# Kernel tuning notes

Measured on AMD Instinct MI355X. Metric: run time of the kernel, lower is better.

## Reference

```python
import jax, jax.numpy as jnp
import numpy as np

N_EMBD = 1024
N_HEAD = 16
HEAD = N_EMBD // N_HEAD


def setup_inputs() -> dict:
    key = jax.random.key(0)
    ks = jax.random.split(key, 5)
    B, T = 2, 2048
    s = 1.0 / np.sqrt(N_EMBD)
    return {
        "x": jax.random.normal(ks[0], (B, T, N_EMBD), jnp.float32),
        "w_attn": jax.random.normal(ks[1], (N_EMBD, 3 * N_EMBD), jnp.float32) * s,
        "b_attn": jnp.zeros((3 * N_EMBD,), jnp.float32),
        "w_proj": jax.random.normal(ks[2], (N_EMBD, N_EMBD), jnp.float32) * s,
        "b_proj": jnp.zeros((N_EMBD,), jnp.float32),
    }


def reference(x, w_attn, b_attn, w_proj, b_proj):
    B, T, C = x.shape
    qkv = x @ w_attn + b_attn                      # [B,T,3C]
    q, k, v = jnp.split(qkv, 3, axis=-1)
    def heads(t):
        return t.reshape(B, T, N_HEAD, HEAD).transpose(0, 2, 1, 3)  # [B,H,T,D]
    q, k, v = heads(q), heads(k), heads(v)
    scale = 1.0 / np.sqrt(HEAD)
    att = jnp.einsum('bhqd,bhkd->bhqk', q, k) * scale
    causal = jnp.tril(jnp.ones((T, T), bool))
    att = jnp.where(causal, att, -jnp.inf)
    p = jax.nn.softmax(att, axis=-1)
    y = jnp.einsum('bhqk,bhkd->bhqd', p, v)        # [B,H,T,D]
    y = y.transpose(0, 2, 1, 3).reshape(B, T, C)
    return y @ w_proj + b_proj
```

## Files before the change

### kernel.cpp

```cpp
#include <hip/hip_runtime.h>
#include <hip/hip_bf16.h>

typedef __attribute__((ext_vector_type(4))) float f32x4;
typedef __attribute__((ext_vector_type(16))) float f32x16;
typedef __attribute__((ext_vector_type(8))) short bf16x8;
typedef __attribute__((ext_vector_type(4))) unsigned int u32x4;

#define MFMA16(a,b,c) __builtin_amdgcn_mfma_f32_16x16x32_bf16(a,b,c,0,0,0)
#define MFMA32(a,b,c) __builtin_amdgcn_mfma_f32_32x32x16_bf16(a,b,c,0,0,0)
#define LOG2E 1.44269504088896340736f

__device__ __forceinline__ float bf2f(unsigned short u){
  unsigned v = ((unsigned)u) << 16;
  float f; __builtin_memcpy(&f, &v, 4); return f;
}
__device__ __forceinline__ unsigned short f2bf(float f){
  unsigned x; __builtin_memcpy(&x, &f, 4);
  x += 0x7fffu + ((x >> 16) & 1u);
  return (unsigned short)(x >> 16);
}
__device__ __forceinline__ void gload_lds16(const void* g, void* l){
  __builtin_amdgcn_global_load_lds((const __attribute__((address_space(1))) void*)g,
                                   (__attribute__((address_space(3))) void*)l, 16, 0, 0);
}
__device__ __forceinline__ f32x16 zero16(){
  f32x16 z;
#pragma unroll
  for (int i = 0; i < 16; ++i) z[i] = 0.f;
  return z;
}
__device__ __forceinline__ unsigned cvtpk(float lo, float hi_){
  unsigned d;
  asm("v_cvt_pk_bf16_f32 %0, %1, %2" : "=v"(d) : "v"(lo), "v"(hi_));
  return d;
}
__device__ __forceinline__ void pack_group(const float* p, bf16x8& f0, bf16x8& f1){
  unsigned a0 = cvtpk(p[0], p[1]),  b0 = cvtpk(p[4],  p[5]);
  unsigned a1 = cvtpk(p[2], p[3]),  b1 = cvtpk(p[6],  p[7]);
  unsigned c0 = cvtpk(p[8], p[9]),  d0 = cvtpk(p[12], p[13]);
  unsigned c1 = cvtpk(p[10],p[11]), d1 = cvtpk(p[14], p[15]);
  asm("v_permlane32_swap_b32 %0, %1" : "+v"(a0), "+v"(b0));
  asm("v_permlane32_swap_b32 %0, %1" : "+v"(a1), "+v"(b1));
  asm("v_permlane32_swap_b32 %0, %1" : "+v"(c0), "+v"(d0));
  asm("v_permlane32_swap_b32 %0, %1" : "+v"(c1), "+v"(d1));
  u32x4 w0 = {a0, a1, b0, b1};
  u32x4 w1 = {c0, c1, d0, d1};
  f0 = __builtin_bit_cast(bf16x8, w0);
  f1 = __builtin_bit_cast(bf16x8, w1);
}

__global__ void k_cast(const float* __restrict__ src, unsigned short* __restrict__ dst){
  const int i = blockIdx.x * 256 + threadIdx.x;
  const float4 v = ((const float4*)src)[i];
  ushort4 o;
  o.x = f2bf(v.x); o.y = f2bf(v.y); o.z = f2bf(v.z); o.w = f2bf(v.w);
  ((ushort4*)dst)[i] = o;
}

__global__ void k_castT(const float* __restrict__ src, unsigned short* __restrict__ dst,
                        const int R, const int C){
  __shared__ unsigned short t[64][65];
  const int r0 = blockIdx.y * 64, c0 = blockIdx.x * 64;
  const int tid = threadIdx.x;
#pragma unroll
  for (int i = 0; i < 16; ++i){
    int idx = i*256 + tid; int r = idx >> 6, c = idx & 63;
    t[r][c] = f2bf(src[(size_t)(r0 + r)*C + c0 + c]);
  }
  __syncthreads();
#pragma unroll
  for (int i = 0; i < 16; ++i){
    int idx = i*256 + tid; int c = idx >> 6, r = idx & 63;
    dst[(size_t)(c0 + c)*R + r0 + r] = t[r][c];
  }
}

__device__ __forceinline__ void gemm_core3(const unsigned short* __restrict__ A,
                                           const unsigned short* __restrict__ Bt,
                                           const int K, const int bm, const int bn,
                                           char* ldsb, f32x4 acc[4][4])
{
  const int tid = threadIdx.x, lane = tid & 63, wave = tid >> 6;
  const int wr = wave >> 1, wc = wave & 1;
  const int l15 = lane & 15, lg = lane >> 4;
  const int o = tid * 16;
  const int srow = o >> 6;
  const int sch = ((o >> 4) & 3) ^ ((srow >> 1) & 3);
  const unsigned short* gA0 = A  + (size_t)(bm + srow)*K      + sch*8;
  const unsigned short* gA1 = A  + (size_t)(bm + 64 + srow)*K + sch*8;
  const unsigned short* gB0 = Bt + (size_t)(bn + srow)*K      + sch*8;
  const unsigned short* gB1 = Bt + (size_t)(bn + 64 + srow)*K + sch*8;
  const int rsw = (l15 >> 1) & 3;
  const int aoff = (wr*64 + l15)*64 + ((lg ^ rsw) << 4);
  const int boff = 8192 + (wc*64 + l15)*64 + ((lg ^ rsw) << 4);

#define STG3(koff, bb) do { \
    gload_lds16(gA0 + (koff), ldsb + (bb) + o); \
    gload_lds16(gA1 + (koff), ldsb + (bb) + 4096 + o); \
    gload_lds16(gB0 + (koff), ldsb + (bb) + 8192 + o); \
    gload_lds16(gB1 + (koff), ldsb + (bb) + 12288 + o); } while(0)

  const int NT = K >> 5;
  STG3(0, 0);
  STG3(32, 16384);
  int bcur = 0, bstg = 32768;
  for (int t = 0; t < NT; ++t){
    if (t + 1 < NT) asm volatile("s_waitcnt vmcnt(4)" ::: "memory");
    else            asm volatile("s_waitcnt vmcnt(0)" ::: "memory");
    __builtin_amdgcn_s_barrier();
    __builtin_amdgcn_sched_barrier(0);
    if (t + 2 < NT) STG3((size_t)(t + 2) << 5, bstg);
    bf16x8 af[4], bg[4];
#pragma unroll
    for (int m = 0; m < 4; ++m) af[m] = *(const bf16x8*)(ldsb + bcur + aoff + m*1024);
#pragma unroll
    for (int n = 0; n < 4; ++n) bg[n] = *(const bf16x8*)(ldsb + bcur + boff + n*1024);
    __builtin_amdgcn_s_setprio(1);
#pragma unroll
    for (int m = 0; m < 4; ++m)
#pragma unroll
      for (int n = 0; n < 4; ++n)
        acc[m][n] = MFMA16(af[m], bg[n], acc[m][n]);
    __builtin_amdgcn_s_setprio(0);
    bcur = (bcur == 32768) ? 0 : bcur + 16384;
    bstg = (bstg == 32768) ? 0 : bstg + 16384;
  }
#undef STG3
}

__global__ __launch_bounds__(256,3) void k_gemm_qkv(const unsigned short* __restrict__ xb,
    const unsigned short* __restrict__ waT, const float* __restrict__ b_attn,
    unsigned short* __restrict__ qb, unsigned short* __restrict__ kb,
    unsigned short* __restrict__ vb)
{
  __shared__ char lds[49152];
  f32x4 acc[4][4];
#pragma unroll
  for (int m = 0; m < 4; ++m)
#pragma unroll
    for (int n = 0; n < 4; ++n) acc[m][n] = (f32x4){0.f,0.f,0.f,0.f};
  int wgid = blockIdx.y * 24 + blockIdx.x;
  wgid = (wgid & 7) * 96 + (wgid >> 3);
  const int bm = (wgid / 24) * 128, bn = (wgid % 24) * 128;
  gemm_core3(xb, waT, 1024, bm, bn, lds, acc);
  const int lane = threadIdx.x & 63, wave = threadIdx.x >> 6;
  const int wr = wave >> 1, wc = wave & 1, l15 = lane & 15, lg = lane >> 4;
#pragma unroll
  for (int m = 0; m < 4; ++m){
#pragma unroll
    for (int n = 0; n < 4; ++n){
#pragma unroll
      for (int r = 0; r < 4; ++r){
        const int row = bm + wr*64 + m*16 + lg*4 + r;
        const int col = bn + wc*64 + n*16 + l15;
        const float val = acc[m][n][r] + b_attn[col];
        const int part = col >> 10, c = col & 1023;
        const int h = c >> 6, d = c & 63;
        const int b = row >> 11, t = row & 2047;
        const unsigned short u = f2bf(val);
        const size_t bhbase = (size_t)(b*16 + h)*131072;
        if (part == 0){
          qb[bhbase + (size_t)t*64 + d] = u;
        } else {
          const int tile = t >> 6, l = t & 63;
          const size_t base = bhbase + (size_t)tile*4096;
          if (part == 1) kb[base + l*64 + ((((d>>3)^(l&7))<<3) | (d&7))] = u;
          else           vb[base + d*64 + ((((l>>3)^(d&7))<<3) | (l&7))] = u;
        }
      }
    }
  }
}

__global__ __launch_bounds__(256,3) void k_gemm_proj(const unsigned short* __restrict__ yb,
    const unsigned short* __restrict__ wpT, const float* __restrict__ b_proj,
    float* __restrict__ out)
{
  __shared__ char lds[49152];
  f32x4 acc[4][4];
#pragma unroll
  for (int m = 0; m < 4; ++m)
#pragma unroll
    for (int n = 0; n < 4; ++n) acc[m][n] = (f32x4){0.f,0.f,0.f,0.f};
  int wgid = blockIdx.y * 8 + blockIdx.x;
  wgid = (wgid & 7) * 32 + (wgid >> 3);
  const int bm = (wgid / 8) * 128, bn = (wgid % 8) * 128;
  gemm_core3(yb, wpT, 1024, bm, bn, lds, acc);
  const int lane = threadIdx.x & 63, wave = threadIdx.x >> 6;
  const int wr = wave >> 1, wc = wave & 1, l15 = lane & 15, lg = lane >> 4;
#pragma unroll
  for (int m = 0; m < 4; ++m){
#pragma unroll
    for (int n = 0; n < 4; ++n){
#pragma unroll
      for (int r = 0; r < 4; ++r){
        const int row = bm + wr*64 + m*16 + lg*4 + r;
        const int col = bn + wc*64 + n*16 + l15;
        out[(size_t)row*1024 + col] = acc[m][n][r] + b_proj[col];
      }
    }
  }
}

__global__ __launch_bounds__(256,2) void k_attn(const unsigned short* __restrict__ q,
                       const unsigned short* __restrict__ kt,
                       const unsigned short* __restrict__ vt,
                       unsigned short* __restrict__ y)
{
  __shared__ char lds[32768];
  const int tid = threadIdx.x, lane = tid & 63, wave = tid >> 6;
  const int l31 = lane & 31, hi = lane >> 5;
  const int i = blockIdx.x, ii = i & 255;
  const int bh = ii & 31;
  const int qbi = (i < 256) ? (15 - (ii >> 5)) : (ii >> 5);
  const int q0w = qbi*128 + wave*32;
  const int ntiles = (qbi + 1) * 2;
  const unsigned short* qh = q + (size_t)bh * 131072;
  const char* kbase = (const char*)(kt + (size_t)bh * 131072);
  const char* vbase = (const char*)(vt + (size_t)bh * 131072);

  const float C = 0.125f * LOG2E;
  const float M = 16.0f;

  bf16x8 qf[4];
  {
    const unsigned short* qp = qh + (size_t)(q0w + l31)*64 + hi*8;
#pragma unroll
    for (int ds = 0; ds < 4; ++ds) qf[ds] = *(const bf16x8*)(qp + ds*16);
  }

  f32x16 yac0 = zero16(), yac1 = zero16();
  float lsum = 0.f;
  const int mask_from = q0w >> 6;
  const int stg = tid * 16;
  const int dst = wave * 1024;
  char* ldsK = lds;
  char* ldsV = lds + 16384;

#define STAGE(tile, buf) do { \
    const char* ks_ = kbase + (size_t)(tile)*8192; \
    const char* vs_ = vbase + (size_t)(tile)*8192; \
    gload_lds16(ks_ + stg,        ldsK + (buf)*8192 + dst); \
    gload_lds16(ks_ + 4096 + stg, ldsK + (buf)*8192 + 4096 + dst); \
    gload_lds16(vs_ + stg,        ldsV + (buf)*8192 + dst); \
    gload_lds16(vs_ + 4096 + stg, ldsV + (buf)*8192 + 4096 + dst); \
  } while(0)

  STAGE(0, 0);
  __syncthreads();

  const int swz = (l31 & 7) << 4;
  const int rowb = l31 * 128;

  for (int t = 0; t < ntiles; ++t){
    const int buf = t & 1;
    if (t + 1 < ntiles) STAGE(t + 1, buf ^ 1);

    const char* kb_ = ldsK + buf*8192;
    const char* vb_ = ldsV + buf*8192;

    bf16x8 kf[8];
#pragma unroll
    for (int ds = 0; ds < 4; ++ds){
      const int ch = ((ds*2 + hi) << 4) ^ swz;
      kf[ds]   = *(const bf16x8*)(kb_ + rowb + ch);
      kf[ds+4] = *(const bf16x8*)(kb_ + 4096 + rowb + ch);
    }
    f32x16 s0 = zero16(), s1 = zero16();
#pragma unroll
    for (int ds = 0; ds < 4; ++ds){
      s0 = MFMA32(kf[ds],   qf[ds], s0);
      s1 = MFMA32(kf[ds+4], qf[ds], s1);
    }

    bf16x8 vf[8];
#pragma unroll
    for (int ks = 0; ks < 4; ++ks){
      const int ch = ((ks*2 + hi) << 4) ^ swz;
      vf[ks]   = *(const bf16x8*)(vb_ + rowb + ch);
      vf[ks+4] = *(const bf16x8*)(vb_ + 4096 + rowb + ch);
    }

    if (t >= mask_from){
      const int qg = q0w + l31, key0 = t << 6;
#pragma unroll
      for (int r = 0; r < 16; ++r){
        const int kl = (r&3) + 8*(r>>2) + 4*hi;
        if (key0 + kl      > qg) s0[r] = -1e30f;
        if (key0 + 32 + kl > qg) s1[r] = -1e30f;
      }
    }

    float p0[16], p1[16];
    float ts = 0.f;
#pragma unroll
    for (int r = 0; r < 16; ++r){
      p0[r] = __builtin_amdgcn_exp2f(__builtin_fmaf(s0[r], C, -M));
      p1[r] = __builtin_amdgcn_exp2f(__builtin_fmaf(s1[r], C, -M));
      ts += p0[r] + p1[r];
    }
    lsum += ts;

    bf16x8 pa[4];
    pack_group(p0, pa[0], pa[1]);
    pack_group(p1, pa[2], pa[3]);
#pragma unroll
    for (int ks = 0; ks < 4; ++ks){
      yac0 = MFMA32(pa[ks], vf[ks],   yac0);
      yac1 = MFMA32(pa[ks], vf[ks+4], yac1);
    }
    __syncthreads();
  }
#undef STAGE

  lsum += __shfl_xor(lsum, 32);
  const float linv = 1.0f / lsum;
  const int b = bh >> 4, h = bh & 15;
  unsigned short* yp = y + ((size_t)b*2048 + q0w)*1024 + h*64;
#pragma unroll
  for (int r = 0; r < 16; ++r){
    const int ql = (r&3) + 8*(r>>2) + 4*hi;
    const float li = __shfl(linv, ql);
    yp[(size_t)ql*1024 + l31]      = f2bf(yac0[r] * li);
    yp[(size_t)ql*1024 + 32 + l31] = f2bf(yac1[r] * li);
  }
}

extern "C" void kernel_launch(void* const* d_in, const int* in_sizes, int n_in,
                              void* d_out, int out_size, void* d_ws, size_t ws_size,
                              hipStream_t stream) {
  const float* x      = (const float*)d_in[0];
  const float* w_attn = (const float*)d_in[1];
  const float* b_attn = (const float*)d_in[2];
  const float* w_proj = (const float*)d_in[3];
  const float* b_proj = (const float*)d_in[4];
  float* out = (float*)d_out;

  unsigned short* ws  = (unsigned short*)d_ws;
  unsigned short* xb  = ws;
  unsigned short* waT = xb  + 4194304;
  unsigned short* wpT = waT + 3145728;
  unsigned short* qb  = wpT + 1048576;
  unsigned short* kb  = qb  + 4194304;
  unsigned short* vb  = kb  + 4194304;
  unsigned short* yb  = vb  + 4194304;

  k_cast<<<dim3(4096), dim3(256), 0, stream>>>(x, xb);
  k_castT<<<dim3(48,16), dim3(256), 0, stream>>>(w_attn, waT, 1024, 3072);
  k_castT<<<dim3(16,16), dim3(256), 0, stream>>>(w_proj, wpT, 1024, 1024);
  k_gemm_qkv<<<dim3(24,32), dim3(256), 0, stream>>>(xb, waT, b_attn, qb, kb, vb);
  k_attn<<<dim3(512), dim3(256), 0, stream>>>(qb, kb, vb, yb);
  k_gemm_proj<<<dim3(8,32), dim3(256), 0, stream>>>(yb, wpT, b_proj, out);
}
```

Measured before the change: 101.0 us.

## Rewrite QKV GEMM with 256x256 tiles, 8 waves, and interleaved staging

Replaces the 128x128 QKV GEMM, which used 4 waves and 3 blocks per CU, with a 256x256 tile computed by 512 threads (8 waves) in 128 KB of LDS with double buffering. Global-to-LDS loads for the next K-tile are split into four pieces and interleaved with the MFMA quarter-phases of the current tile, separated by explicit barriers and waitcnts. The larger tile is meant to raise arithmetic intensity and cut global traffic. In exchange it runs one block per CU with only 192 blocks, so occupancy is lower and some CUs may sit idle.

```diff
diff --git a/kernel.cpp b/kernel.cpp
--- a/kernel.cpp
+++ b/kernel.cpp
@@ -72,6 +72,124 @@
   for (int i = 0; i < 16; ++i){
     int idx = i*256 + tid; int c = idx >> 6, r = idx & 63;
     dst[(size_t)(c0 + c)*R + r0 + r] = t[r][c];
+  }
+}
+
+__global__ __launch_bounds__(512,1) void k_gemm_qkv(const unsigned short* __restrict__ xb,
+    const unsigned short* __restrict__ waT, const float* __restrict__ b_attn,
+    unsigned short* __restrict__ qb, unsigned short* __restrict__ kb,
+    unsigned short* __restrict__ vb)
+{
+  __shared__ char lds[131072];
+  const int K = 1024, NT = 16;
+  const int tid = threadIdx.x, lane = tid & 63, wave = tid >> 6;
+  const int wr = wave >> 2, wc = wave & 3;
+  const int l15 = lane & 15, lg = lane >> 4;
+
+  int h = blockIdx.y * 12 + blockIdx.x;
+  const int wgid = (h & 7) * 24 + (h >> 3);
+  const int bm = (wgid / 12) * 256, bn = (wgid % 12) * 256;
+
+  char* const ldsp = (char*)lds;
+  const int stid = tid * 16;
+  const int srow = stid >> 7;
+  const int sch  = ((stid >> 4) & 7) ^ (srow & 7);
+  const unsigned short* gA = xb  + (size_t)(bm + srow)*K + sch*8;
+  const unsigned short* gB = waT + (size_t)(bn + srow)*K + sch*8;
+  const int rswz = l15 & 7;
+
+  f32x4 acc[8][4];
+#pragma unroll
+  for (int m = 0; m < 8; ++m)
+#pragma unroll
+    for (int n = 0; n < 4; ++n) acc[m][n] = (f32x4){0.f,0.f,0.f,0.f};
+
+#define STAGE_PAIR(T,P,SB) do{ \
+    const unsigned short* g_ = (((P)<2) ? gA : gB) + ((((P)&1)) ? (size_t)128*K : 0) + (size_t)(T)*64; \
+    char* d_ = ldsp + (SB) + (((P)<2) ? 0 : 32768) + ((P)&1)*16384 + stid; \
+    gload_lds16(g_,               d_); \
+    gload_lds16(g_ + (size_t)64*K, d_ + 8192); }while(0)
+
+  STAGE_PAIR(0,0,0); STAGE_PAIR(0,1,0); STAGE_PAIR(0,2,0); STAGE_PAIR(0,3,0);
+
+  bf16x8 aR[4][2], bR[4][2];
+
+#define DSA(MH,CB) _Pragma("unroll") for(int am=0;am<4;++am){ \
+    const int row_ = wr*128 + (MH)*64 + am*16 + l15; \
+    _Pragma("unroll") for(int kh=0;kh<2;++kh) \
+      aR[am][kh] = *(const bf16x8*)(ldsp + (CB) + row_*128 + (((kh*4+lg)^rswz)<<4)); }
+#define DSB(NL,CB) _Pragma("unroll") for(int an=0;an<2;++an){ \
+    const int row_ = wc*64 + ((NL)+an)*16 + l15; \
+    _Pragma("unroll") for(int kh=0;kh<2;++kh) \
+      bR[(NL)+an][kh] = *(const bf16x8*)(ldsp + (CB) + 32768 + row_*128 + (((kh*4+lg)^rswz)<<4)); }
+#define QMFMA(MH,NL) \
+    __builtin_amdgcn_s_setprio(1); \
+    _Pragma("unroll") for(int am=0;am<4;++am) \
+      _Pragma("unroll") for(int an=0;an<2;++an){ \
+        acc[(MH)*4+am][(NL)+an] = MFMA16(aR[am][0], bR[(NL)+an][0], acc[(MH)*4+am][(NL)+an]); \
+        acc[(MH)*4+am][(NL)+an] = MFMA16(aR[am][1], bR[(NL)+an][1], acc[(MH)*4+am][(NL)+an]); } \
+    __builtin_amdgcn_s_setprio(0);
+#define LGKM0 asm volatile("s_waitcnt lgkmcnt(0)":::"memory"); __builtin_amdgcn_sched_barrier(0);
+#define BAR __builtin_amdgcn_s_barrier();
+
+  for (int t = 0; t < NT; ++t){
+    const int cb = (t & 1) << 16;
+    const int sb = cb ^ 65536;
+    if (t + 1 < NT){ STAGE_PAIR(t+1,0,sb); asm volatile("s_waitcnt vmcnt(2)":::"memory"); }
+    else           { asm volatile("s_waitcnt vmcnt(0)":::"memory"); }
+    __builtin_amdgcn_sched_barrier(0);
+    BAR
+    DSA(0,cb); DSB(0,cb);
+    LGKM0
+    QMFMA(0,0)
+    BAR
+    DSB(2,cb);
+    if (t + 1 < NT) STAGE_PAIR(t+1,1,sb);
+    BAR
+    LGKM0
+    QMFMA(0,2)
+    BAR
+    DSA(1,cb);
+    if (t + 1 < NT) STAGE_PAIR(t+1,2,sb);
+    BAR
+    LGKM0
+    QMFMA(1,2)
+    BAR
+    if (t + 1 < NT) STAGE_PAIR(t+1,3,sb);
+    QMFMA(1,0)
+    BAR
+  }
+#undef STAGE_PAIR
+#undef DSA
+#undef DSB
+#undef QMFMA
+#undef LGKM0
+#undef BAR
+
+#pragma unroll
+  for (int am = 0; am < 8; ++am){
+#pragma unroll
+    for (int an = 0; an < 4; ++an){
+#pragma unroll
+      for (int r = 0; r < 4; ++r){
+        const int row = bm + wr*128 + am*16 + lg*4 + r;
+        const int col = bn + wc*64 + an*16 + l15;
+        const float val = acc[am][an][r] + b_attn[col];
+        const int part = col >> 10, c = col & 1023;
+        const int hh = c >> 6, d = c & 63;
+        const int bb = row >> 11, tt = row & 2047;
+        const unsigned short u = f2bf(val);
+        const size_t bhbase = (size_t)(bb*16 + hh)*131072;
+        if (part == 0){
+          qb[bhbase + (size_t)tt*64 + d] = u;
+        } else {
+          const int tile = tt >> 6, l = tt & 63;
+          const size_t base = bhbase + (size_t)tile*4096;
+          if (part == 1) kb[base + l*64 + ((((d>>3)^(l&7))<<3) | (d&7))] = u;
+          else           vb[base + d*64 + ((((l>>3)^(d&7))<<3) | (l&7))] = u;
+        }
+      }
+    }
   }
 }
 
@@ -128,50 +246,6 @@
 #undef STG3
 }
 
-__global__ __launch_bounds__(256,3) void k_gemm_qkv(const unsigned short* __restrict__ xb,
-    const unsigned short* __restrict__ waT, const float* __restrict__ b_attn,
-    unsigned short* __restrict__ qb, unsigned short* __restrict__ kb,
-    unsigned short* __restrict__ vb)
-{
-  __shared__ char lds[49152];
-  f32x4 acc[4][4];
-#pragma unroll
-  for (int m = 0; m < 4; ++m)
-#pragma unroll
-    for (int n = 0; n < 4; ++n) acc[m][n] = (f32x4){0.f,0.f,0.f,0.f};
-  int wgid = blockIdx.y * 24 + blockIdx.x;
-  wgid = (wgid & 7) * 96 + (wgid >> 3);
-  const int bm = (wgid / 24) * 128, bn = (wgid % 24) * 128;
-  gemm_core3(xb, waT, 1024, bm, bn, lds, acc);
-  const int lane = threadIdx.x & 63, wave = threadIdx.x >> 6;
-  const int wr = wave >> 1, wc = wave & 1, l15 = lane & 15, lg = lane >> 4;
-#pragma unroll
-  for (int m = 0; m < 4; ++m){
-#pragma unroll
-    for (int n = 0; n < 4; ++n){
-#pragma unroll
-      for (int r = 0; r < 4; ++r){
-        const int row = bm + wr*64 + m*16 + lg*4 + r;
-        const int col = bn + wc*64 + n*16 + l15;
-        const float val = acc[m][n][r] + b_attn[col];
-        const int part = col >> 10, c = col & 1023;
-        const int h = c >> 6, d = c & 63;
-        const int b = row >> 11, t = row & 2047;
-        const unsigned short u = f2bf(val);
-        const size_t bhbase = (size_t)(b*16 + h)*131072;
-        if (part == 0){
-          qb[bhbase + (size_t)t*64 + d] = u;
-        } else {
-          const int tile = t >> 6, l = t & 63;
-          const size_t base = bhbase + (size_t)tile*4096;
-          if (part == 1) kb[base + l*64 + ((((d>>3)^(l&7))<<3) | (d&7))] = u;
-          else           vb[base + d*64 + ((((l>>3)^(d&7))<<3) | (l&7))] = u;
-        }
-      }
-    }
-  }
-}
-
 __global__ __launch_bounds__(256,3) void k_gemm_proj(const unsigned short* __restrict__ yb,
     const unsigned short* __restrict__ wpT, const float* __restrict__ b_proj,
     float* __restrict__ out)
@@ -348,7 +422,7 @@
   k_cast<<<dim3(4096), dim3(256), 0, stream>>>(x, xb);
   k_castT<<<dim3(48,16), dim3(256), 0, stream>>>(w_attn, waT, 1024, 3072);
   k_castT<<<dim3(16,16), dim3(256), 0, stream>>>(w_proj, wpT, 1024, 1024);
-  k_gemm_qkv<<<dim3(24,32), dim3(256), 0, stream>>>(xb, waT, b_attn, qb, kb, vb);
+  k_gemm_qkv<<<dim3(12,16), dim3(512), 0, stream>>>(xb, waT, b_attn, qb, kb, vb);
   k_attn<<<dim3(512), dim3(256), 0, stream>>>(qb, kb, vb, yb);
   k_gemm_proj<<<dim3(8,32), dim3(256), 0, stream>>>(yb, wpT, b_proj, out);
 }
```

Result: slower. 105.2 us (+4.2%).

## Give each attention wave two query groups to reuse K/V fragments

Applied to the files above, without the earlier changes.

The attention kernel drops from 4 to 2 waves per block, and each wave now handles 64 query rows as two 32-row groups. The K and V fragments read from LDS are shared by both groups, which halves LDS reads per query. Tile staging is spread over fewer threads with more loads each, and waves skip tiles past their own diagonal. The cost is more accumulator registers per wave, fewer waves to hide latency, and possible load imbalance between the two waves on causal tiles.

```diff
diff --git a/kernel.cpp b/kernel.cpp
--- a/kernel.cpp
+++ b/kernel.cpp
@@ -202,7 +202,7 @@
   }
 }
 
-__global__ __launch_bounds__(256,2) void k_attn(const unsigned short* __restrict__ q,
+__global__ __launch_bounds__(128,2) void k_attn(const unsigned short* __restrict__ q,
                        const unsigned short* __restrict__ kt,
                        const unsigned short* __restrict__ vt,
                        unsigned short* __restrict__ y)
@@ -213,8 +213,9 @@
   const int i = blockIdx.x, ii = i & 255;
   const int bh = ii & 31;
   const int qbi = (i < 256) ? (15 - (ii >> 5)) : (ii >> 5);
-  const int q0w = qbi*128 + wave*32;
+  const int qrow0 = qbi*128 + wave*64;
   const int ntiles = (qbi + 1) * 2;
+  const int tb = qrow0 >> 6;
   const unsigned short* qh = q + (size_t)bh * 131072;
   const char* kbase = (const char*)(kt + (size_t)bh * 131072);
   const char* vbase = (const char*)(vt + (size_t)bh * 131072);
@@ -222,28 +223,29 @@
   const float C = 0.125f * LOG2E;
   const float M = 16.0f;
 
-  bf16x8 qf[4];
-  {
-    const unsigned short* qp = qh + (size_t)(q0w + l31)*64 + hi*8;
-#pragma unroll
-    for (int ds = 0; ds < 4; ++ds) qf[ds] = *(const bf16x8*)(qp + ds*16);
-  }
-
-  f32x16 yac0 = zero16(), yac1 = zero16();
-  float lsum = 0.f;
-  const int mask_from = q0w >> 6;
+  bf16x8 qf[2][4];
+#pragma unroll
+  for (int qg = 0; qg < 2; ++qg){
+    const unsigned short* qp = qh + (size_t)(qrow0 + qg*32 + l31)*64 + hi*8;
+#pragma unroll
+    for (int ds = 0; ds < 4; ++ds) qf[qg][ds] = *(const bf16x8*)(qp + ds*16);
+  }
+
+  f32x16 yac[2][2];
+#pragma unroll
+  for (int qg = 0; qg < 2; ++qg){ yac[qg][0] = zero16(); yac[qg][1] = zero16(); }
+  float lsum0 = 0.f, lsum1 = 0.f;
+
   const int stg = tid * 16;
-  const int dst = wave * 1024;
   char* ldsK = lds;
   char* ldsV = lds + 16384;
 
 #define STAGE(tile, buf) do { \
     const char* ks_ = kbase + (size_t)(tile)*8192; \
     const char* vs_ = vbase + (size_t)(tile)*8192; \
-    gload_lds16(ks_ + stg,        ldsK + (buf)*8192 + dst); \
-    gload_lds16(ks_ + 4096 + stg, ldsK + (buf)*8192 + 4096 + dst); \
-    gload_lds16(vs_ + stg,        ldsV + (buf)*8192 + dst); \
-    gload_lds16(vs_ + 4096 + stg, ldsV + (buf)*8192 + 4096 + dst); \
+    _Pragma("unroll") for (int j_ = 0; j_ < 4; ++j_){ \
+      gload_lds16(ks_ + j_*2048 + stg, ldsK + (buf)*8192 + j_*2048 + stg); \
+      gload_lds16(vs_ + j_*2048 + stg, ldsV + (buf)*8192 + j_*2048 + stg); } \
   } while(0)
 
   STAGE(0, 0);
@@ -256,73 +258,86 @@
     const int buf = t & 1;
     if (t + 1 < ntiles) STAGE(t + 1, buf ^ 1);
 
-    const char* kb_ = ldsK + buf*8192;
-    const char* vb_ = ldsV + buf*8192;
-
-    bf16x8 kf[8];
-#pragma unroll
-    for (int ds = 0; ds < 4; ++ds){
-      const int ch = ((ds*2 + hi) << 4) ^ swz;
-      kf[ds]   = *(const bf16x8*)(kb_ + rowb + ch);
-      kf[ds+4] = *(const bf16x8*)(kb_ + 4096 + rowb + ch);
-    }
-    f32x16 s0 = zero16(), s1 = zero16();
-#pragma unroll
-    for (int ds = 0; ds < 4; ++ds){
-      s0 = MFMA32(kf[ds],   qf[ds], s0);
-      s1 = MFMA32(kf[ds+4], qf[ds], s1);
-    }
-
-    bf16x8 vf[8];
-#pragma unroll
-    for (int ks = 0; ks < 4; ++ks){
-      const int ch = ((ks*2 + hi) << 4) ^ swz;
-      vf[ks]   = *(const bf16x8*)(vb_ + rowb + ch);
-      vf[ks+4] = *(const bf16x8*)(vb_ + 4096 + rowb + ch);
-    }
-
-    if (t >= mask_from){
-      const int qg = q0w + l31, key0 = t << 6;
-#pragma unroll
-      for (int r = 0; r < 16; ++r){
-        const int kl = (r&3) + 8*(r>>2) + 4*hi;
-        if (key0 + kl      > qg) s0[r] = -1e30f;
-        if (key0 + 32 + kl > qg) s1[r] = -1e30f;
-      }
-    }
-
-    float p0[16], p1[16];
-    float ts = 0.f;
-#pragma unroll
-    for (int r = 0; r < 16; ++r){
-      p0[r] = __builtin_amdgcn_exp2f(__builtin_fmaf(s0[r], C, -M));
-      p1[r] = __builtin_amdgcn_exp2f(__builtin_fmaf(s1[r], C, -M));
-      ts += p0[r] + p1[r];
-    }
-    lsum += ts;
-
-    bf16x8 pa[4];
-    pack_group(p0, pa[0], pa[1]);
-    pack_group(p1, pa[2], pa[3]);
-#pragma unroll
-    for (int ks = 0; ks < 4; ++ks){
-      yac0 = MFMA32(pa[ks], vf[ks],   yac0);
-      yac1 = MFMA32(pa[ks], vf[ks+4], yac1);
+    if (t <= tb){
+      const char* kb_ = ldsK + buf*8192;
+      const char* vb_ = ldsV + buf*8192;
+
+      bf16x8 kf[8];
+#pragma unroll
+      for (int ds = 0; ds < 4; ++ds){
+        const int ch = ((ds*2 + hi) << 4) ^ swz;
+        kf[ds]   = *(const bf16x8*)(kb_ + rowb + ch);
+        kf[ds+4] = *(const bf16x8*)(kb_ + 4096 + rowb + ch);
+      }
+      f32x16 s[2][2];
+#pragma unroll
+      for (int qg = 0; qg < 2; ++qg){
+        s[qg][0] = zero16(); s[qg][1] = zero16();
+#pragma unroll
+        for (int ds = 0; ds < 4; ++ds){
+          s[qg][0] = MFMA32(kf[ds],   qf[qg][ds], s[qg][0]);
+          s[qg][1] = MFMA32(kf[ds+4], qf[qg][ds], s[qg][1]);
+        }
+      }
+
+      bf16x8 vf[8];
+#pragma unroll
+      for (int ks = 0; ks < 4; ++ks){
+        const int ch = ((ks*2 + hi) << 4) ^ swz;
+        vf[ks]   = *(const bf16x8*)(vb_ + rowb + ch);
+        vf[ks+4] = *(const bf16x8*)(vb_ + 4096 + rowb + ch);
+      }
+
+      const int key0 = t << 6;
+#pragma unroll
+      for (int qg = 0; qg < 2; ++qg){
+        if (t == tb){
+          const int qgl = qrow0 + qg*32 + l31;
+#pragma unroll
+          for (int r = 0; r < 16; ++r){
+            const int kl = (r&3) + 8*(r>>2) + 4*hi;
+            if (key0 + kl      > qgl) s[qg][0][r] = -1e30f;
+            if (key0 + 32 + kl > qgl) s[qg][1][r] = -1e30f;
+          }
+        }
+        float p0[16], p1[16];
+        float ts = 0.f;
+#pragma unroll
+        for (int r = 0; r < 16; ++r){
+          p0[r] = __builtin_amdgcn_exp2f(__builtin_fmaf(s[qg][0][r], C, -M));
+          p1[r] = __builtin_amdgcn_exp2f(__builtin_fmaf(s[qg][1][r], C, -M));
+          ts += p0[r] + p1[r];
+        }
+        if (qg == 0) lsum0 += ts; else lsum1 += ts;
+
+        bf16x8 pa[4];
+        pack_group(p0, pa[0], pa[1]);
+        pack_group(p1, pa[2], pa[3]);
+#pragma unroll
+        for (int ks = 0; ks < 4; ++ks){
+          yac[qg][0] = MFMA32(pa[ks], vf[ks],   yac[qg][0]);
+          yac[qg][1] = MFMA32(pa[ks], vf[ks+4], yac[qg][1]);
+        }
+      }
     }
     __syncthreads();
   }
 #undef STAGE
 
-  lsum += __shfl_xor(lsum, 32);
-  const float linv = 1.0f / lsum;
+  lsum0 += __shfl_xor(lsum0, 32);
+  lsum1 += __shfl_xor(lsum1, 32);
   const int b = bh >> 4, h = bh & 15;
-  unsigned short* yp = y + ((size_t)b*2048 + q0w)*1024 + h*64;
-#pragma unroll
-  for (int r = 0; r < 16; ++r){
-    const int ql = (r&3) + 8*(r>>2) + 4*hi;
-    const float li = __shfl(linv, ql);
-    yp[(size_t)ql*1024 + l31]      = f2bf(yac0[r] * li);
-    yp[(size_t)ql*1024 + 32 + l31] = f2bf(yac1[r] * li);
+#pragma unroll
+  for (int qg = 0; qg < 2; ++qg){
+    const float linv = 1.0f / (qg == 0 ? lsum0 : lsum1);
+    unsigned short* yp = y + ((size_t)b*2048 + qrow0 + qg*32)*1024 + h*64;
+#pragma unroll
+    for (int r = 0; r < 16; ++r){
+      const int ql = (r&3) + 8*(r>>2) + 4*hi;
+      const float li = __shfl(linv, ql);
+      yp[(size_t)ql*1024 + l31]      = f2bf(yac[qg][0][r] * li);
+      yp[(size_t)ql*1024 + 32 + l31] = f2bf(yac[qg][1][r] * li);
+    }
   }
 }
 
@@ -349,6 +364,6 @@
   k_castT<<<dim3(48,16), dim3(256), 0, stream>>>(w_attn, waT, 1024, 3072);
   k_castT<<<dim3(16,16), dim3(256), 0, stream>>>(w_proj, wpT, 1024, 1024);
   k_gemm_qkv<<<dim3(24,32), dim3(256), 0, stream>>>(xb, waT, b_attn, qb, kb, vb);
-  k_attn<<<dim3(512), dim3(256), 0, stream>>>(qb, kb, vb, yb);
+  k_attn<<<dim3(512), dim3(128), 0, stream>>>(qb, kb, vb, yb);
   k_gemm_proj<<<dim3(8,32), dim3(256), 0, stream>>>(yb, wpT, b_proj, out);
 }
```

After: 115.6 us. 14.5% more time.
